# Kernel tuning notes

Measured on AMD Instinct MI355X. Metric: run time of the kernel, lower is better.

Reference implementation:

```python
import jax, jax.numpy as jnp
import numpy as np
from jax import lax

B, C_IN, L = 32, 64, 8192
PF = 128


def caudil_conv(x, W, kw, dilation, causal_padding=0):
    """x: (B, C, L); W: (O, kw*C) with layout W[o, c*kw + j] (channel-major).
    Equivalent to the per-timestep sliced-Linear loop: VALID dilated conv."""
    C = x.shape[1]
    if causal_padding:
        x = jnp.pad(x, ((0, 0), (0, 0), (causal_padding, 0)))
    K = W.reshape(-1, C, kw)  # (O, C, kw)
    return lax.conv_general_dilated(
        x, K, window_strides=(1,), padding='VALID', rhs_dilation=(dilation,),
        dimension_numbers=('NCH', 'OIH', 'NCH'))


def setup_inputs() -> dict:
    key = jax.random.key(0)
    ks = jax.random.split(key, 10)
    s = lambda k, shp: (jax.random.normal(k, shp, dtype=jnp.float32) * 0.05)
    return {
        'x': jax.random.normal(ks[0], (B, C_IN, L), dtype=jnp.float32),
        'w7_1': s(ks[1], (6, 3 * C_IN)),
        'w7_3': s(ks[2], (PF, 3 * 6)),
        'w10_1': s(ks[3], (6, 3 * C_IN)),
        'w10_3': s(ks[4], (6, 3 * 6)),
        'w10_5': s(ks[5], (PF, 2 * 6)),
        'w15_1': s(ks[6], (6, 3 * C_IN)),
        'w15_3': s(ks[7], (6, 3 * 6)),
        'w15_5': s(ks[8], (PF, 3 * 6)),
    }


def reference(x, w7_1, w7_3, w10_1, w10_3, w10_5, w15_1, w15_3, w15_5):
    relu = jax.nn.relu
    # branch 7: (3,d1) -> (3,d2)
    m7 = relu(caudil_conv(x, w7_1, 3, 1))
    m7 = relu(caudil_conv(m7, w7_3, 3, 2))
    # branch 10: (3,d1) -> (3,d2) -> (2,d4,pad4)
    m10 = relu(caudil_conv(x, w10_1, 3, 1))
    m10 = relu(caudil_conv(m10, w10_3, 3, 2))
    m10 = relu(caudil_conv(m10, w10_5, 2, 4, causal_padding=4))
    # branch 15: (3,d1) -> (3,d2) -> (3,d4,pad8)
    m15 = relu(caudil_conv(x, w15_1, 3, 1))
    m15 = relu(caudil_conv(m15, w15_3, 3, 2))
    m15 = relu(caudil_conv(m15, w15_5, 3, 4, causal_padding=8))
    return jnp.concatenate([m7, m10, m15], axis=1)  # (B, 3*PF, L-6)
```

## Files before the change

### kernel.cpp

```cpp
#include <hip/hip_runtime.h>

constexpr int Bn   = 32;
constexpr int CIN  = 64;
constexpr int Lx   = 8192;
constexpr int L1   = 8190;
constexpr int LOUT = 8186;
constexpr int NCH  = 384;

constexpr int WS1_OFF = 0;
constexpr int H_OFF   = 4096;
constexpr int HSTR    = 8208;

__global__ void prep_weights(const float* __restrict__ w7_1,
                             const float* __restrict__ w10_1,
                             const float* __restrict__ w15_1,
                             float* __restrict__ ws) {
    int idx = blockIdx.x * blockDim.x + threadIdx.x;
    if (idx >= 64 * 54) return;
    int ci = idx / 54, r = idx % 54;
    int k = r / 3, j = r % 3;
    const float* src = (k < 6) ? w7_1 : ((k < 12) ? w10_1 : w15_1);
    int kk = (k < 6) ? k : ((k < 12) ? k - 6 : k - 12);
    ws[WS1_OFF + ci * 64 + r] = src[kk * 192 + ci * 3 + j];
}

constexpr int TTA = 252;
constexpr int NTA = (L1 + TTA - 1) / TTA;

__global__ __launch_bounds__(256)
void stage12(const float* __restrict__ x, float* __restrict__ ws,
             const float* __restrict__ w10_3, const float* __restrict__ w15_3) {
    __shared__ float a2[12][256];
    const int tid = threadIdx.x;
    const int t0  = blockIdx.x * TTA;
    const int b   = blockIdx.y;
    const float* xb = x + (size_t)b * CIN * Lx;
    float* hb = ws + H_OFF + (size_t)b * 18 * HSTR;

    if (blockIdx.x == 0 && tid < 18 * 8)
        hb[(tid >> 3) * HSTR + (tid & 7)] = 0.f;

    const int s = t0 + tid;
    float acc[18];
    #pragma unroll
    for (int k = 0; k < 18; ++k) acc[k] = 0.f;
    if (s < L1) {
        const float* xr = xb + s;
        const float* w0 = ws + WS1_OFF;
        for (int ci = 0; ci < CIN; ++ci) {
            const float x0 = xr[0];
            const float x1 = xr[1];
            const float x2 = xr[2];
            const float* wr = w0 + ci * 64;
            #pragma unroll
            for (int k = 0; k < 18; ++k) {
                acc[k] = fmaf(wr[k * 3 + 0], x0, acc[k]);
                acc[k] = fmaf(wr[k * 3 + 1], x1, acc[k]);
                acc[k] = fmaf(wr[k * 3 + 2], x2, acc[k]);
            }
            xr += Lx;
        }
        #pragma unroll
        for (int k = 0; k < 18; ++k) acc[k] = fmaxf(acc[k], 0.f);
        if (tid < TTA) {
            #pragma unroll
            for (int c = 0; c < 6; ++c) hb[c * HSTR + 8 + s] = acc[c];
        }
    }
    #pragma unroll
    for (int c = 0; c < 12; ++c) a2[c][tid] = acc[6 + c];
    __syncthreads();

    const int u = t0 + tid;
    if (tid < TTA && u < LOUT) {
        float v[18];
        #pragma unroll
        for (int c = 0; c < 6; ++c)
            #pragma unroll
            for (int j = 0; j < 3; ++j) v[c * 3 + j] = a2[c][tid + 2 * j];
        #pragma unroll
        for (int k = 0; k < 6; ++k) {
            float a = 0.f;
            #pragma unroll
            for (int r = 0; r < 18; ++r) a = fmaf(w10_3[k * 18 + r], v[r], a);
            hb[(6 + k) * HSTR + 8 + u] = fmaxf(a, 0.f);
        }
        #pragma unroll
        for (int c = 0; c < 6; ++c)
            #pragma unroll
            for (int j = 0; j < 3; ++j) v[c * 3 + j] = a2[6 + c][tid + 2 * j];
        #pragma unroll
        for (int k = 0; k < 6; ++k) {
            float a = 0.f;
            #pragma unroll
            for (int r = 0; r < 18; ++r) a = fmaf(w15_3[k * 18 + r], v[r], a);
            hb[(12 + k) * HSTR + 8 + u] = fmaxf(a, 0.f);
        }
    }
}

constexpr int TTB = 512;
constexpr int NTB = 16;

__device__ __forceinline__ void store8(float* __restrict__ op, int t,
                                       float* __restrict__ a) {
    #pragma unroll
    for (int d = 0; d < 8; ++d) a[d] = fmaxf(a[d], 0.f);
    if (t + 7 < LOUT) {
        #pragma unroll
        for (int d = 0; d < 8; d += 2)
            *(float2*)(op + t + d) = make_float2(a[d], a[d + 1]);
    } else {
        #pragma unroll
        for (int d = 0; d < 8; ++d)
            if (t + d < LOUT) op[t + d] = a[d];
    }
}

__global__ __launch_bounds__(256)
void stage3(const float* __restrict__ ws,
            const float* __restrict__ w7_3,
            const float* __restrict__ w10_5,
            const float* __restrict__ w15_5,
            float* __restrict__ out) {
    __shared__ float hs[6][528];
    const int tid = threadIdx.x;
    const int t0  = blockIdx.x * TTB;
    const int br  = blockIdx.y;
    const int b   = blockIdx.z;
    const float* hb = ws + H_OFF + ((size_t)b * 18 + br * 6) * HSTR;

    for (int idx = tid; idx < 6 * 132; idx += 256) {
        const int c = idx / 132, q = idx - c * 132;
        *(float4*)&hs[c][q * 4] = *(const float4*)&hb[c * HSTR + t0 + q * 4];
    }
    __syncthreads();

    const int tq  = tid & 63;
    const int wvU = __builtin_amdgcn_readfirstlane(threadIdx.x >> 6);
    const int t   = t0 + tq * 8;
    const int rel = tq * 8;

    if (br == 0) {
        float v[6][12];
        #pragma unroll
        for (int c = 0; c < 6; ++c)
            #pragma unroll
            for (int m = 0; m < 12; m += 4)
                *(float4*)&v[c][m] = *(const float4*)&hs[c][rel + 8 + m];
        const float* wb = w7_3 + wvU * 32 * 18;
        float* ob = out + ((size_t)b * NCH + wvU * 32) * LOUT;
        #pragma unroll 2
        for (int oi = 0; oi < 32; ++oi) {
            const float* wr = wb + oi * 18;
            float a[8];
            #pragma unroll
            for (int d = 0; d < 8; ++d) a[d] = 0.f;
            #pragma unroll
            for (int c = 0; c < 6; ++c)
                #pragma unroll
                for (int j = 0; j < 3; ++j) {
                    const float w = wr[c * 3 + j];
                    #pragma unroll
                    for (int d = 0; d < 8; ++d) a[d] = fmaf(w, v[c][d + 2 * j], a[d]);
                }
            store8(ob + (size_t)oi * LOUT, t, a);
        }
    } else if (br == 1) {
        float v[6][12];
        #pragma unroll
        for (int c = 0; c < 6; ++c)
            #pragma unroll
            for (int m = 0; m < 12; m += 4)
                *(float4*)&v[c][m] = *(const float4*)&hs[c][rel + 4 + m];
        const float* wb = w10_5 + wvU * 32 * 12;
        float* ob = out + ((size_t)b * NCH + 128 + wvU * 32) * LOUT;
        #pragma unroll 2
        for (int oi = 0; oi < 32; ++oi) {
            const float* wr = wb + oi * 12;
            float a[8];
            #pragma unroll
            for (int d = 0; d < 8; ++d) a[d] = 0.f;
            #pragma unroll
            for (int c = 0; c < 6; ++c) {
                const float w0 = wr[c * 2 + 0];
                const float w1 = wr[c * 2 + 1];
                #pragma unroll
                for (int d = 0; d < 8; ++d) {
                    a[d] = fmaf(w0, v[c][d], a[d]);
                    a[d] = fmaf(w1, v[c][d + 4], a[d]);
                }
            }
            store8(ob + (size_t)oi * LOUT, t, a);
        }
    } else {
        float v[6][16];
        #pragma unroll
        for (int c = 0; c < 6; ++c)
            #pragma unroll
            for (int m = 0; m < 16; m += 4)
                *(float4*)&v[c][m] = *(const float4*)&hs[c][rel + m];
        const float* wb = w15_5 + wvU * 32 * 18;
        float* ob = out + ((size_t)b * NCH + 256 + wvU * 32) * LOUT;
        #pragma unroll 2
        for (int oi = 0; oi < 32; ++oi) {
            const float* wr = wb + oi * 18;
            float a[8];
            #pragma unroll
            for (int d = 0; d < 8; ++d) a[d] = 0.f;
            #pragma unroll
            for (int c = 0; c < 6; ++c)
                #pragma unroll
                for (int j = 0; j < 3; ++j) {
                    const float w = wr[c * 3 + j];
                    #pragma unroll
                    for (int d = 0; d < 8; ++d) a[d] = fmaf(w, v[c][d + 4 * j], a[d]);
                }
            store8(ob + (size_t)oi * LOUT, t, a);
        }
    }
}

extern "C" void kernel_launch(void* const* d_in, const int* in_sizes, int n_in,
                              void* d_out, int out_size, void* d_ws, size_t ws_size,
                              hipStream_t stream) {
    const float* x     = (const float*)d_in[0];
    const float* w7_1  = (const float*)d_in[1];
    const float* w7_3  = (const float*)d_in[2];
    const float* w10_1 = (const float*)d_in[3];
    const float* w10_3 = (const float*)d_in[4];
    const float* w10_5 = (const float*)d_in[5];
    const float* w15_1 = (const float*)d_in[6];
    const float* w15_3 = (const float*)d_in[7];
    const float* w15_5 = (const float*)d_in[8];
    float* out = (float*)d_out;
    float* ws  = (float*)d_ws;

    prep_weights<<<dim3(14), dim3(256), 0, stream>>>(w7_1, w10_1, w15_1, ws);
    stage12<<<dim3(NTA, Bn), dim3(256), 0, stream>>>(x, ws, w10_3, w15_3);
    stage3<<<dim3(NTB, 3, Bn), dim3(256), 0, stream>>>(ws, w7_3, w10_5, w15_5, out);
}
```

Baseline: 643.2 us.

## Remap stage3 threads to two timesteps each across all 128 output channels

Stage3 previously had each wave own 32 output channels, with each lane computing 8 consecutive timesteps. Now each thread computes 2 consecutive timesteps for all 128 output channels. Adjacent lanes therefore write contiguous float2s, so each output row store is fully coalesced across the wave. The trade-off is less register reuse of the input window per weight load, and four times as many scalar weight loads per thread.

```diff
diff --git a/kernel.cpp b/kernel.cpp
--- a/kernel.cpp
+++ b/kernel.cpp
@@ -102,21 +102,6 @@
 constexpr int TTB = 512;
 constexpr int NTB = 16;
 
-__device__ __forceinline__ void store8(float* __restrict__ op, int t,
-                                       float* __restrict__ a) {
-    #pragma unroll
-    for (int d = 0; d < 8; ++d) a[d] = fmaxf(a[d], 0.f);
-    if (t + 7 < LOUT) {
-        #pragma unroll
-        for (int d = 0; d < 8; d += 2)
-            *(float2*)(op + t + d) = make_float2(a[d], a[d + 1]);
-    } else {
-        #pragma unroll
-        for (int d = 0; d < 8; ++d)
-            if (t + d < LOUT) op[t + d] = a[d];
-    }
-}
-
 __global__ __launch_bounds__(256)
 void stage3(const float* __restrict__ ws,
             const float* __restrict__ w7_3,
@@ -136,87 +121,79 @@
     }
     __syncthreads();
 
-    const int tq  = tid & 63;
-    const int wvU = __builtin_amdgcn_readfirstlane(threadIdx.x >> 6);
-    const int t   = t0 + tq * 8;
-    const int rel = tq * 8;
+    const int rel = 2 * tid;
+    const int t   = t0 + rel;
+    const bool ok = (t < LOUT);
 
     if (br == 0) {
-        float v[6][12];
-        #pragma unroll
-        for (int c = 0; c < 6; ++c)
-            #pragma unroll
-            for (int m = 0; m < 12; m += 4)
-                *(float4*)&v[c][m] = *(const float4*)&hs[c][rel + 8 + m];
-        const float* wb = w7_3 + wvU * 32 * 18;
-        float* ob = out + ((size_t)b * NCH + wvU * 32) * LOUT;
-        #pragma unroll 2
-        for (int oi = 0; oi < 32; ++oi) {
-            const float* wr = wb + oi * 18;
-            float a[8];
-            #pragma unroll
-            for (int d = 0; d < 8; ++d) a[d] = 0.f;
+        float v[6][6];
+        #pragma unroll
+        for (int c = 0; c < 6; ++c)
+            #pragma unroll
+            for (int k = 0; k < 6; ++k) v[c][k] = hs[c][rel + 8 + k];
+        float* ob = out + (size_t)b * NCH * LOUT;
+        #pragma unroll 4
+        for (int oi = 0; oi < 128; ++oi) {
+            const float* wr = w7_3 + oi * 18;
+            float a0 = 0.f, a1 = 0.f;
             #pragma unroll
             for (int c = 0; c < 6; ++c)
                 #pragma unroll
                 for (int j = 0; j < 3; ++j) {
                     const float w = wr[c * 3 + j];
-                    #pragma unroll
-                    for (int d = 0; d < 8; ++d) a[d] = fmaf(w, v[c][d + 2 * j], a[d]);
+                    a0 = fmaf(w, v[c][2 * j], a0);
+                    a1 = fmaf(w, v[c][2 * j + 1], a1);
                 }
-            store8(ob + (size_t)oi * LOUT, t, a);
+            if (ok)
+                *(float2*)(ob + (size_t)oi * LOUT + t) =
+                    make_float2(fmaxf(a0, 0.f), fmaxf(a1, 0.f));
         }
     } else if (br == 1) {
-        float v[6][12];
-        #pragma unroll
-        for (int c = 0; c < 6; ++c)
-            #pragma unroll
-            for (int m = 0; m < 12; m += 4)
-                *(float4*)&v[c][m] = *(const float4*)&hs[c][rel + 4 + m];
-        const float* wb = w10_5 + wvU * 32 * 12;
-        float* ob = out + ((size_t)b * NCH + 128 + wvU * 32) * LOUT;
-        #pragma unroll 2
-        for (int oi = 0; oi < 32; ++oi) {
-            const float* wr = wb + oi * 12;
-            float a[8];
-            #pragma unroll
-            for (int d = 0; d < 8; ++d) a[d] = 0.f;
+        float v[6][6];
+        #pragma unroll
+        for (int c = 0; c < 6; ++c)
+            #pragma unroll
+            for (int k = 0; k < 6; ++k) v[c][k] = hs[c][rel + 4 + k];
+        float* ob = out + ((size_t)b * NCH + 128) * LOUT;
+        #pragma unroll 4
+        for (int oi = 0; oi < 128; ++oi) {
+            const float* wr = w10_5 + oi * 12;
+            float a0 = 0.f, a1 = 0.f;
             #pragma unroll
             for (int c = 0; c < 6; ++c) {
                 const float w0 = wr[c * 2 + 0];
                 const float w1 = wr[c * 2 + 1];
-                #pragma unroll
-                for (int d = 0; d < 8; ++d) {
-                    a[d] = fmaf(w0, v[c][d], a[d]);
-                    a[d] = fmaf(w1, v[c][d + 4], a[d]);
-                }
+                a0 = fmaf(w0, v[c][0], a0);
+                a1 = fmaf(w0, v[c][1], a1);
+                a0 = fmaf(w1, v[c][4], a0);
+                a1 = fmaf(w1, v[c][5], a1);
             }
-            store8(ob + (size_t)oi * LOUT, t, a);
+            if (ok)
+                *(float2*)(ob + (size_t)oi * LOUT + t) =
+                    make_float2(fmaxf(a0, 0.f), fmaxf(a1, 0.f));
         }
     } else {
-        float v[6][16];
-        #pragma unroll
-        for (int c = 0; c < 6; ++c)
-            #pragma unroll
-            for (int m = 0; m < 16; m += 4)
-                *(float4*)&v[c][m] = *(const float4*)&hs[c][rel + m];
-        const float* wb = w15_5 + wvU * 32 * 18;
-        float* ob = out + ((size_t)b * NCH + 256 + wvU * 32) * LOUT;
-        #pragma unroll 2
-        for (int oi = 0; oi < 32; ++oi) {
-            const float* wr = wb + oi * 18;
-            float a[8];
-            #pragma unroll
-            for (int d = 0; d < 8; ++d) a[d] = 0.f;
+        float v[6][10];
+        #pragma unroll
+        for (int c = 0; c < 6; ++c)
+            #pragma unroll
+            for (int k = 0; k < 10; ++k) v[c][k] = hs[c][rel + k];
+        float* ob = out + ((size_t)b * NCH + 256) * LOUT;
+        #pragma unroll 4
+        for (int oi = 0; oi < 128; ++oi) {
+            const float* wr = w15_5 + oi * 18;
+            float a0 = 0.f, a1 = 0.f;
             #pragma unroll
             for (int c = 0; c < 6; ++c)
                 #pragma unroll
                 for (int j = 0; j < 3; ++j) {
                     const float w = wr[c * 3 + j];
-                    #pragma unroll
-                    for (int d = 0; d < 8; ++d) a[d] = fmaf(w, v[c][d + 4 * j], a[d]);
+                    a0 = fmaf(w, v[c][4 * j], a0);
+                    a1 = fmaf(w, v[c][4 * j + 1], a1);
                 }
-            store8(ob + (size_t)oi * LOUT, t, a);
+            if (ok)
+                *(float2*)(ob + (size_t)oi * LOUT + t) =
+                    make_float2(fmaxf(a0, 0.f), fmaxf(a1, 0.f));
         }
     }
 }
```

New measurement: 650.6 us. No clear change (+1.2%).
